# Optimization experiments

Measured on AMD Instinct MI355X. Metric: run time of the kernel, lower is better.

The kernel has to match this reference:

```python
import jax, jax.numpy as jnp
import numpy as np

N = 262144        # number of rows (mesh nodes)
E = 2_000_000     # random off-diagonal pairs (symmetrized)
F = 4             # n_feature (columns of b)
RTOL = 1e-5
ATOL = 0.0
MAXITER = 100


def setup_inputs() -> dict:
    rng = np.random.default_rng(0)
    r = rng.integers(0, N, E)
    c = rng.integers(0, N, E)
    w = (rng.random(E) + 0.1).astype(np.float32)
    # symmetric diagonally-dominant matrix: Laplacian(w) + I  (SPD)
    row = np.concatenate([r, c, np.arange(N)]).astype(np.int32)
    col = np.concatenate([c, r, np.arange(N)]).astype(np.int32)
    deg = np.zeros(N, np.float32)
    np.add.at(deg, r, w)
    np.add.at(deg, c, w)
    vals = np.concatenate([-w, -w, deg + 1.0]).astype(np.float32)
    key = jax.random.key(0)
    b = jax.random.normal(key, (N, F), dtype=jnp.float32)
    return {
        "values": jnp.asarray(vals),
        "b": b,
        "row": jnp.asarray(row),
        "col": jnp.asarray(col),
    }


def _cg(values, row, col, rhs):
    """Batched CG solve of A x = rhs where A is COO (row, col, values).

    batch_solve=True semantics: the [n, f] unknown is treated as one long
    vector; dot products reduce over all n*f elements (as in the wrapped
    scipy LinearOperator of size (n*f, n*f)).
    """
    n = rhs.shape[0]

    def spmv(v):  # v: [n, f] -> [n, f]
        return jax.ops.segment_sum(values[:, None] * v[col], row, num_segments=n)

    bnorm = jnp.sqrt(jnp.sum(rhs * rhs))
    tol = jnp.maximum(RTOL * bnorm, ATOL)

    x0 = jnp.zeros_like(rhs)
    r0 = rhs  # b - A @ 0
    state = (x0, r0, r0, jnp.sum(r0 * r0), jnp.int32(0))

    def cond(s):
        _, _, _, rho, k = s
        return (jnp.sqrt(rho) > tol) & (k < MAXITER)

    def body(s):
        x, r, p, rho, k = s
        q = spmv(p)
        alpha = rho / jnp.sum(p * q)
        x = x + alpha * p
        r = r - alpha * q
        rho_new = jnp.sum(r * r)
        p = r + (rho_new / rho) * p
        return (x, r, p, rho_new, k + 1)

    x, _, _, _, _ = jax.lax.while_loop(cond, body, state)
    return x


def reference(values, b, row, col):
    return _cg(values, row, col, b)
```

## Files before the change

kernel.cpp:

```cpp
#include <hip/hip_runtime.h>

#define NT 1024
#define NB 256
#define MAXIT 100
#define RTOL_F 1e-5f

typedef float f4 __attribute__((ext_vector_type(4)));

__device__ __forceinline__ unsigned long long pk2(float a, float b) {
    return ((unsigned long long)__float_as_uint(b) << 32) | (unsigned long long)__float_as_uint(a);
}

__device__ __forceinline__ void ld16_cc(const f4* a, f4& d) {
    asm volatile("global_load_dwordx4 %0, %1, off sc0 sc1" : "=v"(d) : "v"(a));
}
__device__ __forceinline__ void wait16x8(f4& a, f4& b, f4& c, f4& d,
                                         f4& e, f4& f, f4& g, f4& h) {
    asm volatile("s_waitcnt vmcnt(0)"
                 : "+v"(a), "+v"(b), "+v"(c), "+v"(d),
                   "+v"(e), "+v"(f), "+v"(g), "+v"(h));
}
__device__ __forceinline__ void st16_cc(f4* a, f4 v) {
    asm volatile("global_store_dwordx4 %0, %1, off sc0 sc1" :: "v"(a), "v"(v) : "memory");
}

__device__ __forceinline__ void fbar(int* flags, int seq) {
    __syncthreads();
    if (threadIdx.x == 0)
        __hip_atomic_store(&flags[blockIdx.x], seq, __ATOMIC_RELAXED, __HIP_MEMORY_SCOPE_AGENT);
    if (threadIdx.x < 64) {
        const int b4 = threadIdx.x << 2;
        for (;;) {
            const int f0 = __hip_atomic_load(&flags[b4 + 0], __ATOMIC_RELAXED, __HIP_MEMORY_SCOPE_AGENT);
            const int f1 = __hip_atomic_load(&flags[b4 + 1], __ATOMIC_RELAXED, __HIP_MEMORY_SCOPE_AGENT);
            const int f2 = __hip_atomic_load(&flags[b4 + 2], __ATOMIC_RELAXED, __HIP_MEMORY_SCOPE_AGENT);
            const int f3 = __hip_atomic_load(&flags[b4 + 3], __ATOMIC_RELAXED, __HIP_MEMORY_SCOPE_AGENT);
            const bool ok = (f0 >= seq) && (f1 >= seq) && (f2 >= seq) && (f3 >= seq);
            if (__all(ok)) break;
            __builtin_amdgcn_s_sleep(1);
        }
    }
    __syncthreads();
}

__device__ __forceinline__ void fbar_heavy(int* flags, int seq) {
    __builtin_amdgcn_fence(__ATOMIC_RELEASE, "agent");
    fbar(flags, seq);
    __builtin_amdgcn_fence(__ATOMIC_ACQUIRE, "agent");
}

__device__ __forceinline__ float2 block_sum2_bcast(float a, float b, float* smf) {
#pragma unroll
    for (int o = 32; o > 0; o >>= 1) { a += __shfl_down(a, o); b += __shfl_down(b, o); }
    __syncthreads();
    const int w = threadIdx.x >> 6;
    if ((threadIdx.x & 63) == 0) { smf[w] = a; smf[16 + w] = b; }
    __syncthreads();
    float ra = 0.f, rb = 0.f;
#pragma unroll
    for (int i = 0; i < 16; ++i) { ra += smf[i]; rb += smf[16 + i]; }
    return make_float2(ra, rb);
}

__device__ __forceinline__ float2 sum_parts2(const unsigned long long* buf, float* smf) {
    float a = 0.f, b = 0.f;
    if (threadIdx.x < NB) {
        unsigned long long u = __hip_atomic_load(&buf[threadIdx.x], __ATOMIC_RELAXED,
                                                 __HIP_MEMORY_SCOPE_AGENT);
        a = __uint_as_float((unsigned)(u & 0xffffffffu));
        b = __uint_as_float((unsigned)(u >> 32));
    }
    return block_sum2_bcast(a, b, smf);
}

__device__ __forceinline__ int block_incl_scan(int v, int* smi) {
    const int t = threadIdx.x;
    smi[t] = v;
    __syncthreads();
    for (int off = 1; off < NT; off <<= 1) {
        int add = (t >= off) ? smi[t - off] : 0;
        __syncthreads();
        v += add;
        smi[t] = v;
        __syncthreads();
    }
    return v;
}

__device__ __forceinline__ f4 spmv_row(const long long* __restrict__ bp0, int c,
                                       const f4* __restrict__ rq) {
    f4 a4 = {0.f, 0.f, 0.f, 0.f};
    for (int j = 0; j < c; j += 8) {
        long long e[8];
#pragma unroll
        for (int u = 0; u < 8; ++u) e[u] = bp0[(j + u) * 64];
        f4 g0, g1, g2, g3, g4, g5, g6, g7;
        ld16_cc(rq + (int)(e[0] & 0xffffffffLL), g0);
        ld16_cc(rq + (int)(e[1] & 0xffffffffLL), g1);
        ld16_cc(rq + (int)(e[2] & 0xffffffffLL), g2);
        ld16_cc(rq + (int)(e[3] & 0xffffffffLL), g3);
        ld16_cc(rq + (int)(e[4] & 0xffffffffLL), g4);
        ld16_cc(rq + (int)(e[5] & 0xffffffffLL), g5);
        ld16_cc(rq + (int)(e[6] & 0xffffffffLL), g6);
        ld16_cc(rq + (int)(e[7] & 0xffffffffLL), g7);
        wait16x8(g0, g1, g2, g3, g4, g5, g6, g7);
        a4 += __int_as_float((int)(e[0] >> 32)) * g0;
        a4 += __int_as_float((int)(e[1] >> 32)) * g1;
        a4 += __int_as_float((int)(e[2] >> 32)) * g2;
        a4 += __int_as_float((int)(e[3] >> 32)) * g3;
        a4 += __int_as_float((int)(e[4] >> 32)) * g4;
        a4 += __int_as_float((int)(e[5] >> 32)) * g5;
        a4 += __int_as_float((int)(e[6] >> 32)) * g6;
        a4 += __int_as_float((int)(e[7] >> 32)) * g7;
    }
    return a4;
}

__global__ void __launch_bounds__(NT, 4)
cg_solver_kernel(const float* __restrict__ values,
                 const f4* __restrict__ bvec,
                 const int* __restrict__ rowi,
                 const int* __restrict__ coli,
                 f4* __restrict__ x,
                 f4* __restrict__ wA,
                 f4* __restrict__ wB,
                 int* __restrict__ counts,
                 int* __restrict__ ridx,
                 int* __restrict__ jarr,
                 int* __restrict__ soff,
                 unsigned long long* __restrict__ part,
                 int* __restrict__ flags,
                 long long* __restrict__ sell,
                 int n, int nnz, int nslice)
{
    const int t = threadIdx.x;
    const int tid = blockIdx.x * NT + t;
    const int nth = gridDim.x * NT;
    __shared__ int smi[NT];
    __shared__ float smf[32];
    int seq = 0;

    for (int i = tid; i < n; i += nth) { counts[i] = 0; ridx[i] = 0; }
    fbar_heavy(flags, ++seq);

    for (int e = tid; e < nnz; e += nth) atomicAdd(&counts[rowi[e]], 1);
    f4 rv = bvec[tid];
    st16_cc(&wB[tid], rv);
    fbar_heavy(flags, ++seq);

    for (int s = tid; s < nslice; s += nth) {
        const int rb = s << 6;
        int m = 0;
#pragma unroll 4
        for (int i = 0; i < 64; ++i) m = max(m, counts[rb + i]);
        jarr[s] = (m + 7) & ~7;
    }
    fbar_heavy(flags, ++seq);

    if (blockIdx.x == 0) {
        const int spt = (nslice + NT - 1) / NT;
        const int base = t * spt;
        int local = 0;
        for (int i = 0; i < spt; ++i) {
            int s = base + i;
            if (s < nslice) local += 64 * jarr[s];
        }
        int incl = block_incl_scan(local, smi);
        int run = incl - local;
        for (int i = 0; i < spt; ++i) {
            int s = base + i;
            if (s < nslice) { soff[s] = run; run += 64 * jarr[s]; }
        }
        if (t == NT - 1) soff[nslice] = incl;
    }
    fbar_heavy(flags, ++seq);

    {
        const int total = soff[nslice];
        for (int i = tid; i < total; i += nth) sell[i] = 0LL;
    }
    fbar_heavy(flags, ++seq);

    for (int e = tid; e < nnz; e += nth) {
        const int rr = rowi[e];
        const int i = atomicAdd(&ridx[rr], 1);
        const int pos = soff[rr >> 6] + (i << 6) + (rr & 63);
        sell[pos] = ((long long)__float_as_int(values[e]) << 32) | (unsigned int)coli[e];
    }
    fbar_heavy(flags, ++seq);

    const int wid = tid >> 6;
    const int lane = t & 63;
    const long long* __restrict__ bp0 = sell + soff[wid] + lane;
    const int c = (counts[tid] + 7) & ~7;

    f4 pv = {0.f, 0.f, 0.f, 0.f};
    f4 sv = {0.f, 0.f, 0.f, 0.f};
    f4 zv = {0.f, 0.f, 0.f, 0.f};
    f4 xv = {0.f, 0.f, 0.f, 0.f};
    f4 wv;

    {
        wv = spmv_row(bp0, c, wB);
        st16_cc(&wA[tid], wv);
        float g_p = rv.x * rv.x + rv.y * rv.y + rv.z * rv.z + rv.w * rv.w;
        float d_p = rv.x * wv.x + rv.y * wv.y + rv.z * wv.z + rv.w * wv.w;
        float2 tot = block_sum2_bcast(g_p, d_p, smf);
        if (t == 0)
            __hip_atomic_store(&part[blockIdx.x], pk2(tot.x, tot.y), __ATOMIC_RELAXED, __HIP_MEMORY_SCOPE_AGENT);
    }
    fbar(flags, ++seq);

    float tol2 = 0.f;
    float rho_prev = 1.f;
    float alpha = 1.f;

    for (int k = 0;; ++k) {
        float2 rm = sum_parts2(part + (k & 1) * NB, smf);
        if (k == 0) tol2 = RTOL_F * RTOL_F * rm.x;
        if (!(rm.x > tol2 && k < MAXIT)) break;
        const float beta = (k == 0) ? 0.f : rm.x / rho_prev;
        alpha = rm.x / (rm.y - beta * rm.x / alpha);
        rho_prev = rm.x;

        const f4* wq = (k & 1) ? wB : wA;
        f4 qv = spmv_row(bp0, c, wq);

        zv = qv + beta * zv;
        sv = wv + beta * sv;
        pv = rv + beta * pv;
        xv = xv + alpha * pv;
        rv = rv - alpha * sv;
        wv = wv - alpha * zv;

        f4* wt = (k & 1) ? wA : wB;
        st16_cc(&wt[tid], wv);
        {
            float g_p = rv.x * rv.x + rv.y * rv.y + rv.z * rv.z + rv.w * rv.w;
            float d_p = rv.x * wv.x + rv.y * wv.y + rv.z * wv.z + rv.w * wv.w;
            float2 tot = block_sum2_bcast(g_p, d_p, smf);
            if (t == 0)
                __hip_atomic_store(&part[((k + 1) & 1) * NB + blockIdx.x], pk2(tot.x, tot.y),
                                   __ATOMIC_RELAXED, __HIP_MEMORY_SCOPE_AGENT);
        }
        fbar(flags, ++seq);
    }

    x[tid] = xv;
}

extern "C" void kernel_launch(void* const* d_in, const int* in_sizes, int n_in,
                              void* d_out, int out_size, void* d_ws, size_t ws_size,
                              hipStream_t stream) {
    const float* values = (const float*)d_in[0];
    const f4* bvec      = (const f4*)d_in[1];
    const int* rowi     = (const int*)d_in[2];
    const int* coli     = (const int*)d_in[3];
    const int nnz = in_sizes[0];
    const int n   = in_sizes[1] / 4;
    const int nslice = n / 64;

    char* ws = (char*)d_ws;
    size_t off = 0;
    auto alloc = [&](size_t bytes) -> void* {
        off = (off + 255) & ~(size_t)255;
        void* pp = ws + off;
        off += bytes;
        return pp;
    };
    int* flags   = (int*)alloc((size_t)NB * 4);
    f4* wA       = (f4*)alloc((size_t)n * 16);
    f4* wB       = (f4*)alloc((size_t)n * 16);
    unsigned long long* part = (unsigned long long*)alloc((size_t)2 * NB * 8);
    int* counts  = (int*)alloc((size_t)n * 4);
    int* ridx    = (int*)alloc((size_t)n * 4);
    int* jarr    = (int*)alloc((size_t)nslice * 4);
    int* soff    = (int*)alloc((size_t)(nslice + 1) * 4);
    off = (off + 255) & ~(size_t)255;
    long long* sell = (long long*)(ws + off);
    f4* x = (f4*)d_out;

    hipMemsetAsync(flags, 0, (size_t)NB * 4, stream);

    int n_ = n, nnz_ = nnz, nslice_ = nslice;
    void* args[] = {
        (void*)&values, (void*)&bvec, (void*)&rowi, (void*)&coli,
        (void*)&x, (void*)&wA, (void*)&wB,
        (void*)&counts, (void*)&ridx, (void*)&jarr, (void*)&soff,
        (void*)&part, (void*)&flags,
        (void*)&sell, (void*)&n_, (void*)&nnz_, (void*)&nslice_
    };
    hipLaunchCooperativeKernel((void*)cg_solver_kernel, dim3(NB), dim3(NT),
                               args, 0, stream);
}
```

Baseline: 1.838 ms.

## Add Jacobi preconditioning to the pipelined CG solver

Builds the matrix diagonal during SELL construction and turns the pipelined CG recurrence into Jacobi-preconditioned pipelined CG. This adds the u/q/m vectors, a third reduction for the residual norm, and stores the preconditioned vector for the SpMV. The aim is fewer iterations, since iteration count dominates runtime. In exchange each iteration carries a few more vector ops and a wider reduction, setup gains one barrier, and the iterates no longer match unpreconditioned CG exactly, though the result still converges within tolerance.

```diff
diff --git a/kernel.cpp b/kernel.cpp
--- a/kernel.cpp
+++ b/kernel.cpp
@@ -9,6 +9,9 @@
 
 __device__ __forceinline__ unsigned long long pk2(float a, float b) {
     return ((unsigned long long)__float_as_uint(b) << 32) | (unsigned long long)__float_as_uint(a);
+}
+__device__ __forceinline__ float dot4(f4 a, f4 b) {
+    return a.x * b.x + a.y * b.y + a.z * b.z + a.w * b.w;
 }
 
 __device__ __forceinline__ void ld16_cc(const f4* a, f4& d) {
@@ -49,28 +52,33 @@
     __builtin_amdgcn_fence(__ATOMIC_ACQUIRE, "agent");
 }
 
-__device__ __forceinline__ float2 block_sum2_bcast(float a, float b, float* smf) {
+__device__ __forceinline__ float3 block_sum3_bcast(float a, float b, float c, float* smf) {
 #pragma unroll
-    for (int o = 32; o > 0; o >>= 1) { a += __shfl_down(a, o); b += __shfl_down(b, o); }
+    for (int o = 32; o > 0; o >>= 1) {
+        a += __shfl_down(a, o); b += __shfl_down(b, o); c += __shfl_down(c, o);
+    }
     __syncthreads();
     const int w = threadIdx.x >> 6;
-    if ((threadIdx.x & 63) == 0) { smf[w] = a; smf[16 + w] = b; }
-    __syncthreads();
-    float ra = 0.f, rb = 0.f;
+    if ((threadIdx.x & 63) == 0) { smf[w] = a; smf[16 + w] = b; smf[32 + w] = c; }
+    __syncthreads();
+    float ra = 0.f, rb = 0.f, rc = 0.f;
 #pragma unroll
-    for (int i = 0; i < 16; ++i) { ra += smf[i]; rb += smf[16 + i]; }
-    return make_float2(ra, rb);
-}
-
-__device__ __forceinline__ float2 sum_parts2(const unsigned long long* buf, float* smf) {
-    float a = 0.f, b = 0.f;
+    for (int i = 0; i < 16; ++i) { ra += smf[i]; rb += smf[16 + i]; rc += smf[32 + i]; }
+    return make_float3(ra, rb, rc);
+}
+
+__device__ __forceinline__ float3 sum_parts3(const unsigned long long* buf, float* smf) {
+    float a = 0.f, b = 0.f, c = 0.f;
     if (threadIdx.x < NB) {
-        unsigned long long u = __hip_atomic_load(&buf[threadIdx.x], __ATOMIC_RELAXED,
-                                                 __HIP_MEMORY_SCOPE_AGENT);
-        a = __uint_as_float((unsigned)(u & 0xffffffffu));
-        b = __uint_as_float((unsigned)(u >> 32));
-    }
-    return block_sum2_bcast(a, b, smf);
+        unsigned long long u1 = __hip_atomic_load(&buf[threadIdx.x], __ATOMIC_RELAXED,
+                                                  __HIP_MEMORY_SCOPE_AGENT);
+        unsigned long long u2 = __hip_atomic_load(&buf[NB + threadIdx.x], __ATOMIC_RELAXED,
+                                                  __HIP_MEMORY_SCOPE_AGENT);
+        a = __uint_as_float((unsigned)(u1 & 0xffffffffu));
+        b = __uint_as_float((unsigned)(u1 >> 32));
+        c = __uint_as_float((unsigned)(u2 & 0xffffffffu));
+    }
+    return block_sum3_bcast(a, b, c, smf);
 }
 
 __device__ __forceinline__ int block_incl_scan(int v, int* smi) {
@@ -130,6 +138,7 @@
                  int* __restrict__ soff,
                  unsigned long long* __restrict__ part,
                  int* __restrict__ flags,
+                 float* __restrict__ diag,
                  long long* __restrict__ sell,
                  int n, int nnz, int nslice)
 {
@@ -137,15 +146,14 @@
     const int tid = blockIdx.x * NT + t;
     const int nth = gridDim.x * NT;
     __shared__ int smi[NT];
-    __shared__ float smf[32];
+    __shared__ float smf[48];
     int seq = 0;
 
-    for (int i = tid; i < n; i += nth) { counts[i] = 0; ridx[i] = 0; }
+    for (int i = tid; i < n; i += nth) { counts[i] = 0; ridx[i] = 0; diag[i] = 0.f; }
     fbar_heavy(flags, ++seq);
 
     for (int e = tid; e < nnz; e += nth) atomicAdd(&counts[rowi[e]], 1);
     f4 rv = bvec[tid];
-    st16_cc(&wB[tid], rv);
     fbar_heavy(flags, ++seq);
 
     for (int s = tid; s < nslice; s += nth) {
@@ -185,7 +193,10 @@
         const int rr = rowi[e];
         const int i = atomicAdd(&ridx[rr], 1);
         const int pos = soff[rr >> 6] + (i << 6) + (rr & 63);
-        sell[pos] = ((long long)__float_as_int(values[e]) << 32) | (unsigned int)coli[e];
+        const int cc = coli[e];
+        const float vv = values[e];
+        sell[pos] = ((long long)__float_as_int(vv) << 32) | (unsigned int)cc;
+        if (cc == rr) atomicAdd(&diag[rr], vv);
     }
     fbar_heavy(flags, ++seq);
 
@@ -193,55 +204,67 @@
     const int lane = t & 63;
     const long long* __restrict__ bp0 = sell + soff[wid] + lane;
     const int c = (counts[tid] + 7) & ~7;
+    const float invd = 1.0f / diag[tid];
 
     f4 pv = {0.f, 0.f, 0.f, 0.f};
     f4 sv = {0.f, 0.f, 0.f, 0.f};
     f4 zv = {0.f, 0.f, 0.f, 0.f};
+    f4 qv = {0.f, 0.f, 0.f, 0.f};
     f4 xv = {0.f, 0.f, 0.f, 0.f};
-    f4 wv;
+    f4 uv, wv, mv;
+
+    uv = invd * rv;
+    st16_cc(&wB[tid], uv);
+    fbar(flags, ++seq);
 
     {
         wv = spmv_row(bp0, c, wB);
-        st16_cc(&wA[tid], wv);
-        float g_p = rv.x * rv.x + rv.y * rv.y + rv.z * rv.z + rv.w * rv.w;
-        float d_p = rv.x * wv.x + rv.y * wv.y + rv.z * wv.z + rv.w * wv.w;
-        float2 tot = block_sum2_bcast(g_p, d_p, smf);
-        if (t == 0)
+        mv = invd * wv;
+        st16_cc(&wA[tid], mv);
+        float3 tot = block_sum3_bcast(dot4(rv, uv), dot4(wv, uv), dot4(rv, rv), smf);
+        if (t == 0) {
             __hip_atomic_store(&part[blockIdx.x], pk2(tot.x, tot.y), __ATOMIC_RELAXED, __HIP_MEMORY_SCOPE_AGENT);
+            __hip_atomic_store(&part[NB + blockIdx.x], pk2(tot.z, 0.f), __ATOMIC_RELAXED, __HIP_MEMORY_SCOPE_AGENT);
+        }
     }
     fbar(flags, ++seq);
 
     float tol2 = 0.f;
-    float rho_prev = 1.f;
+    float gamma_prev = 1.f;
     float alpha = 1.f;
 
     for (int k = 0;; ++k) {
-        float2 rm = sum_parts2(part + (k & 1) * NB, smf);
-        if (k == 0) tol2 = RTOL_F * RTOL_F * rm.x;
-        if (!(rm.x > tol2 && k < MAXIT)) break;
-        const float beta = (k == 0) ? 0.f : rm.x / rho_prev;
+        float3 rm = sum_parts3(part + (k & 1) * 2 * NB, smf);
+        if (k == 0) tol2 = RTOL_F * RTOL_F * rm.z;
+        if (!(rm.z > tol2 && k < MAXIT)) break;
+        const float beta = (k == 0) ? 0.f : rm.x / gamma_prev;
         alpha = rm.x / (rm.y - beta * rm.x / alpha);
-        rho_prev = rm.x;
+        gamma_prev = rm.x;
 
         const f4* wq = (k & 1) ? wB : wA;
-        f4 qv = spmv_row(bp0, c, wq);
-
-        zv = qv + beta * zv;
+        f4 nv = spmv_row(bp0, c, wq);
+
+        zv = nv + beta * zv;
+        qv = mv + beta * qv;
         sv = wv + beta * sv;
-        pv = rv + beta * pv;
+        pv = uv + beta * pv;
         xv = xv + alpha * pv;
         rv = rv - alpha * sv;
+        uv = uv - alpha * qv;
         wv = wv - alpha * zv;
+        mv = invd * wv;
 
         f4* wt = (k & 1) ? wA : wB;
-        st16_cc(&wt[tid], wv);
+        st16_cc(&wt[tid], mv);
         {
-            float g_p = rv.x * rv.x + rv.y * rv.y + rv.z * rv.z + rv.w * rv.w;
-            float d_p = rv.x * wv.x + rv.y * wv.y + rv.z * wv.z + rv.w * wv.w;
-            float2 tot = block_sum2_bcast(g_p, d_p, smf);
-            if (t == 0)
-                __hip_atomic_store(&part[((k + 1) & 1) * NB + blockIdx.x], pk2(tot.x, tot.y),
+            float3 tot = block_sum3_bcast(dot4(rv, uv), dot4(wv, uv), dot4(rv, rv), smf);
+            if (t == 0) {
+                const int base = ((k + 1) & 1) * 2 * NB;
+                __hip_atomic_store(&part[base + blockIdx.x], pk2(tot.x, tot.y),
                                    __ATOMIC_RELAXED, __HIP_MEMORY_SCOPE_AGENT);
+                __hip_atomic_store(&part[base + NB + blockIdx.x], pk2(tot.z, 0.f),
+                                   __ATOMIC_RELAXED, __HIP_MEMORY_SCOPE_AGENT);
+            }
         }
         fbar(flags, ++seq);
     }
@@ -271,11 +294,12 @@
     int* flags   = (int*)alloc((size_t)NB * 4);
     f4* wA       = (f4*)alloc((size_t)n * 16);
     f4* wB       = (f4*)alloc((size_t)n * 16);
-    unsigned long long* part = (unsigned long long*)alloc((size_t)2 * NB * 8);
+    unsigned long long* part = (unsigned long long*)alloc((size_t)4 * NB * 8);
     int* counts  = (int*)alloc((size_t)n * 4);
     int* ridx    = (int*)alloc((size_t)n * 4);
     int* jarr    = (int*)alloc((size_t)nslice * 4);
     int* soff    = (int*)alloc((size_t)(nslice + 1) * 4);
+    float* diag  = (float*)alloc((size_t)n * 4);
     off = (off + 255) & ~(size_t)255;
     long long* sell = (long long*)(ws + off);
     f4* x = (f4*)d_out;
@@ -287,7 +311,7 @@
         (void*)&values, (void*)&bvec, (void*)&rowi, (void*)&coli,
         (void*)&x, (void*)&wA, (void*)&wB,
         (void*)&counts, (void*)&ridx, (void*)&jarr, (void*)&soff,
-        (void*)&part, (void*)&flags,
+        (void*)&part, (void*)&flags, (void*)&diag,
         (void*)&sell, (void*)&n_, (void*)&nnz_, (void*)&nslice_
     };
     hipLaunchCooperativeKernel((void*)cg_solver_kernel, dim3(NB), dim3(NT),
```

New measurement: 1.561 ms. 1.18x faster.
